# Performance work log

Hardware: AMD Instinct MI355X
Metric: run time of the kernel (lower is better)

Reference implementation:

```python
import jax, jax.numpy as jnp
from jax import lax
import numpy as np

B, W, V, E, H = 512, 40, 12000, 512, 512


def setup_inputs() -> dict:
    key = jax.random.key(0)
    ks = jax.random.split(key, 9)
    s = 0.05
    ques_vec = jax.random.randint(ks[0], (B, W), 0, V + 1)          # token ids, 0 = pad
    ques_len = jax.random.randint(ks[1], (B,), 1, W + 1)             # valid lengths in [1, W]
    lookup_W = jax.random.normal(ks[2], (E, V), jnp.float32) * s     # nn.Linear(vocab, emb).weight
    wih0 = jax.random.normal(ks[3], (2, 4 * H, E), jnp.float32) * s  # [dir, 4H, in]
    whh0 = jax.random.normal(ks[4], (2, 4 * H, H), jnp.float32) * s
    b0 = jax.random.normal(ks[5], (2, 2, 4 * H), jnp.float32) * s    # [dir, {b_ih,b_hh}, 4H]
    wih1 = jax.random.normal(ks[6], (2, 4 * H, 2 * H), jnp.float32) * s
    whh1 = jax.random.normal(ks[7], (2, 4 * H, H), jnp.float32) * s
    b1 = jax.random.normal(ks[8], (2, 2, 4 * H), jnp.float32) * s
    return {"ques_vec": ques_vec, "ques_len": ques_len, "lookup_W": lookup_W,
            "wih0": wih0, "whh0": whh0, "b0": b0,
            "wih1": wih1, "whh1": whh1, "b1": b1}


def _lstm_dir(x, wih, whh, b, reverse):
    # x: [B, T, D]; PyTorch gate order i, f, g, o
    Hc = whh.shape[1]
    xg = jnp.einsum('btd,gd->btg', x, wih) + b[0] + b[1]  # [B, T, 4H]
    xs = jnp.swapaxes(xg, 0, 1)                            # [T, B, 4H]
    if reverse:
        xs = xs[::-1]

    def step(carry, g_t):
        h, c = carry
        g = g_t + h @ whh.T
        i, f, gg, o = jnp.split(g, 4, axis=-1)
        c = jax.nn.sigmoid(f) * c + jax.nn.sigmoid(i) * jnp.tanh(gg)
        h = jax.nn.sigmoid(o) * jnp.tanh(c)
        return (h, c), h

    h0 = jnp.zeros((x.shape[0], Hc), x.dtype)
    _, hs = lax.scan(step, (h0, h0), xs)
    if reverse:
        hs = hs[::-1]
    return jnp.swapaxes(hs, 0, 1)  # [B, T, H]


def _bilstm(x, wih, whh, b):
    fwd = _lstm_dir(x, wih[0], whh[0], b[0], False)
    bwd = _lstm_dir(x, wih[1], whh[1], b[1], True)
    return jnp.concatenate([fwd, bwd], axis=-1)  # [B, T, 2H]


def reference(ques_vec, ques_len, lookup_W, wih0, whh0, b0, wih1, whh1, b1):
    # one-hot over vocab+1 with column 0 dropped == gather with id 0 -> zero vector
    table = jnp.concatenate([jnp.zeros((1, E), lookup_W.dtype), lookup_W.T], axis=0)  # [V+1, E]
    emb = jnp.tanh(table[ques_vec])          # [B, W, E] (dropout=0 -> identity)
    h = _bilstm(emb, wih0, whh0, b0)         # layer 0
    h = _bilstm(h, wih1, whh1, b1)           # layer 1 -> [B, W, 2H]
    # scatter-mask bmm == select hidden state at timestep ques_len-1
    idx = (ques_len - 1)[:, None, None]
    return jnp.take_along_axis(h, idx, axis=1).reshape(ques_vec.shape[0], -1)  # [B, 2H]
```

## Files before the change

### kernel.cpp

```cpp
#include <hip/hip_runtime.h>
#include <hip/hip_bf16.h>
#include <stdint.h>

#define NB 512
#define NW 40
#define NE 512
#define NH 512
#define NV 12000
#define G4 2048

typedef unsigned short u16;
typedef unsigned int u32;
typedef unsigned long long u64;
typedef __attribute__((ext_vector_type(8))) short short8;
typedef __attribute__((ext_vector_type(4))) float f32x4;

__device__ __forceinline__ unsigned short f2bf(float f) {
  unsigned int u = __float_as_uint(f);
  u += 0x7FFF + ((u >> 16) & 1);
  return (unsigned short)(u >> 16);
}
__device__ __forceinline__ float bf2f(unsigned short b) {
  return __uint_as_float(((unsigned int)b) << 16);
}
__device__ __forceinline__ float loadIn(const void* p, long i, int bf) {
  return bf ? bf2f(((const u16*)p)[i]) : ((const float*)p)[i];
}
__device__ __forceinline__ float fast_tanh(float x) {
  float ax = __builtin_fabsf(x);
  float t = 1.f - 2.f * __builtin_amdgcn_rcpf(__expf(ax + ax) + 1.f);
  return __builtin_copysignf(t, x);
}
__device__ __forceinline__ float sigm(float x) {
  return __builtin_amdgcn_rcpf(1.f + __expf(-x));
}

__global__ void detect_kernel(const u16* p, int* flag) {
  __shared__ int cnt;
  int i = threadIdx.x;
  if (i == 0) cnt = 0;
  __syncthreads();
  unsigned short u = p[2 * (i * 1001)];
  int e = (u >> 7) & 0xFF;
  if (e >= 100 && e <= 126) atomicAdd(&cnt, 1);
  __syncthreads();
  if (i == 0) *flag = (cnt >= 32) ? 1 : 0;
}

__global__ void table_kernel(const void* lookup, const int* flag, u16* tableT) {
  __shared__ float tile[64][65];
  int bf = *flag;
  int v0 = blockIdx.x * 64, e0 = blockIdx.y * 64;
  int tx = threadIdx.x, ty = threadIdx.y;
#pragma unroll
  for (int r = 0; r < 16; ++r) {
    int e = r * 4 + ty, v = tx;
    if (v0 + v < NV)
      tile[e][v] = tanhf(loadIn(lookup, (long)(e0 + e) * NV + v0 + v, bf));
  }
  __syncthreads();
#pragma unroll
  for (int r = 0; r < 16; ++r) {
    int v = r * 4 + ty, e = tx;
    if (v0 + v < NV)
      tableT[(long)(v0 + v) * NE + e0 + e] = f2bf(tile[e][v]);
  }
}

__global__ void pack_kernel(const void* wih0, const void* whh0, const void* b0,
                            const void* wih1, const void* whh1, const void* b1,
                            const int* flag, u16* Wc0, u16* Wc1, float* bsum,
                            u16* G) {
  const long N0 = 2L * G4 * 1024, N1 = 2L * G4 * 1536;
  const long NB2 = 2L * 2 * G4;
  long idx = (long)blockIdx.x * 256 + threadIdx.x;
  int bf = *flag;
  if (idx < N0) {
    int d = (int)(idx / (G4 * 1024));
    int rem = (int)(idx % (long)(G4 * 1024));
    int g = rem / 1024, k = rem % 1024;
    float v = (k < 512) ? loadIn(wih0, ((long)d * G4 + g) * 512 + k, bf)
                        : loadIn(whh0, ((long)d * G4 + g) * 512 + (k - 512), bf);
    Wc0[idx] = f2bf(v);
  } else if (idx < N0 + N1) {
    long i2 = idx - N0;
    int d = (int)(i2 / (G4 * 1536));
    int rem = (int)(i2 % (long)(G4 * 1536));
    int g = rem / 1536, k = rem % 1536;
    float v = (k < 1024) ? loadIn(wih1, ((long)d * G4 + g) * 1024 + k, bf)
                         : loadIn(whh1, ((long)d * G4 + g) * 512 + (k - 1024), bf);
    Wc1[i2] = f2bf(v);
  } else if (idx < N0 + N1 + NB2) {
    long i3 = idx - N0 - N1;
    int layer = (int)(i3 / (2 * G4));
    int d = (int)((i3 / G4) & 1);
    int g = (int)(i3 % G4);
    const void* bb = layer ? b1 : b0;
    float v = loadIn(bb, (long)d * 2 * G4 + g, bf) +
              loadIn(bb, (long)d * 2 * G4 + G4 + g, bf);
    bsum[i3] = v;
  } else if (idx < N0 + N1 + NB2 + 4096) {
    int n = (int)(idx - N0 - N1 - NB2);
    int d = n >> 11, loc = n & 2047;
    int colb = loc >> 7, rr = loc & 127;
    int jn = rr >> 2, g = rr & 3;
    int grow = g * 512 + colb * 32 + jn;
    float v = loadIn(b0, (long)d * 2 * G4 + grow, bf) +
              loadIn(b0, (long)d * 2 * G4 + G4 + grow, bf);
    G[n] = f2bf(v);
  }
}

__global__ void zero_bar(unsigned int* bar) {
  bar[blockIdx.x * 256 + threadIdx.x] = 0u;
}

__global__ __launch_bounds__(256, 3) void g_gemm(
    const u16* __restrict__ tableT, const u16* __restrict__ Wc,
    const float* __restrict__ bsumL, u16* __restrict__ G) {
  __shared__ __align__(16) char lds[32768];
  const int tid = threadIdx.x;
  const int lane = tid & 63, wv = tid >> 6;
  const int wm = wv & 1, wn = wv >> 1;
  const int col = lane & 15, quad = lane >> 4;
  const int bx = blockIdx.x >> 5;
  const int by = blockIdx.x & 31;
  const int tb0 = bx * 128;
  const int d = by >> 4, colb = by & 15, j0 = colb * 32;

  f32x4 zero = {0.f, 0.f, 0.f, 0.f};
  f32x4 acc[4][4];
#pragma unroll
  for (int i = 0; i < 4; ++i)
#pragma unroll
    for (int j = 0; j < 4; ++j) acc[i][j] = zero;

  for (int it = 0; it < 8; ++it) {
    int k0 = it << 6;
#pragma unroll
    for (int p = 0; p < 8; ++p) {
      int c = p * 256 + tid;
      const u16* gsrc;
      if (c < 1024) {
        int r = c >> 3, sl = c & 7;
        int kk = k0 + ((sl * 8) ^ ((r & 7) << 3));
        gsrc = tableT + (long)(tb0 + r) * 512 + kk;
      } else {
        int cb = c - 1024;
        int r = cb >> 3, sl = cb & 7;
        int kk = k0 + ((sl * 8) ^ ((r & 7) << 3));
        int grow = (r >> 5) * 512 + j0 + (r & 31);
        gsrc = Wc + ((long)d * G4 + grow) * 1024 + kk;
      }
      __builtin_amdgcn_global_load_lds(
          (const __attribute__((address_space(1))) void*)(const void*)gsrc,
          (__attribute__((address_space(3))) void*)(lds + p * 4096 + wv * 1024),
          16, 0, 0);
    }
    __syncthreads();
    const u16* As = (const u16*)lds;
    const u16* Bs = (const u16*)(lds + 16384);
#pragma unroll
    for (int ks = 0; ks < 2; ++ks) {
      short8 afr[4], bfr[4];
#pragma unroll
      for (int mf = 0; mf < 4; ++mf) {
        int rm = wm * 64 + mf * 16 + col;
        int sl = (ks * 32 + quad * 8) ^ ((rm & 7) << 3);
        afr[mf] = *(const short8*)(As + rm * 64 + sl);
      }
#pragma unroll
      for (int nf = 0; nf < 4; ++nf) {
        int br = wn * 64 + nf * 16 + col;
        int sl = (ks * 32 + quad * 8) ^ ((br & 7) << 3);
        bfr[nf] = *(const short8*)(Bs + br * 64 + sl);
      }
#pragma unroll
      for (int mf = 0; mf < 4; ++mf)
#pragma unroll
        for (int nf = 0; nf < 4; ++nf)
          acc[mf][nf] = __builtin_amdgcn_mfma_f32_16x16x32_bf16(
              afr[mf], bfr[nf], acc[mf][nf], 0, 0, 0);
    }
    __syncthreads();
  }

  float bias[4];
#pragma unroll
  for (int nf = 0; nf < 4; ++nf) {
    int n = wn * 64 + nf * 16 + col;
    bias[nf] = bsumL[d * G4 + (n >> 5) * 512 + j0 + (n & 31)];
  }
#pragma unroll
  for (int mf = 0; mf < 4; ++mf)
#pragma unroll
    for (int nf = 0; nf < 4; ++nf) {
      int n = wn * 64 + nf * 16 + col;
      int g = n >> 5, jn = n & 31;
#pragma unroll
      for (int r = 0; r < 4; ++r) {
        int m = wm * 64 + mf * 16 + quad * 4 + r;
        int v = tb0 + m;
        if (v < NV)
          G[(long)(v + 1) * 4096 + ((d * 16 + colb) << 7) + jn * 4 + g] =
              f2bf(acc[mf][nf][r] + bias[nf]);
      }
    }
}

__global__ __launch_bounds__(256, 3) void xg_gemm(
    const u16* __restrict__ X, int Kx, int Kfull, const u16* __restrict__ Wc,
    const float* __restrict__ bsumL, u16* __restrict__ xg) {
  __shared__ __align__(16) char lds[32768];
  const int tid = threadIdx.x;
  const int lane = tid & 63, wv = tid >> 6;
  const int wm = wv & 1, wn = wv >> 1;
  const int col = lane & 15, quad = lane >> 4;
  const int s = blockIdx.x >> 5, w = blockIdx.x & 31;
  const int bx = (s % 40) * 4 + (w & 3);
  const int by = (s / 40) * 8 + (w >> 2);
  const int tb0 = bx * 128;
  const int d = by >> 4, colb = by & 15, j0 = colb * 32;

  f32x4 zero = {0.f, 0.f, 0.f, 0.f};
  f32x4 acc[4][4];
#pragma unroll
  for (int i = 0; i < 4; ++i)
#pragma unroll
    for (int j = 0; j < 4; ++j) acc[i][j] = zero;

  const int iters = Kx >> 6;
  for (int it = 0; it < iters; ++it) {
    int k0 = it << 6;
#pragma unroll
    for (int p = 0; p < 8; ++p) {
      int c = p * 256 + tid;
      const u16* gsrc;
      if (c < 1024) {
        int r = c >> 3, sl = c & 7;
        int kk = k0 + ((sl * 8) ^ ((r & 7) << 3));
        gsrc = X + (long)(tb0 + r) * Kx + kk;
      } else {
        int cb = c - 1024;
        int r = cb >> 3, sl = cb & 7;
        int kk = k0 + ((sl * 8) ^ ((r & 7) << 3));
        int grow = (r >> 5) * 512 + j0 + (r & 31);
        gsrc = Wc + ((long)d * G4 + grow) * Kfull + kk;
      }
      __builtin_amdgcn_global_load_lds(
          (const __attribute__((address_space(1))) void*)(const void*)gsrc,
          (__attribute__((address_space(3))) void*)(lds + p * 4096 + wv * 1024),
          16, 0, 0);
    }
    __syncthreads();
    const u16* As = (const u16*)lds;
    const u16* Bs = (const u16*)(lds + 16384);
#pragma unroll
    for (int ks = 0; ks < 2; ++ks) {
      short8 afr[4], bfr[4];
#pragma unroll
      for (int mf = 0; mf < 4; ++mf) {
        int rm = wm * 64 + mf * 16 + col;
        int sl = (ks * 32 + quad * 8) ^ ((rm & 7) << 3);
        afr[mf] = *(const short8*)(As + rm * 64 + sl);
      }
#pragma unroll
      for (int nf = 0; nf < 4; ++nf) {
        int br = wn * 64 + nf * 16 + col;
        int sl = (ks * 32 + quad * 8) ^ ((br & 7) << 3);
        bfr[nf] = *(const short8*)(Bs + br * 64 + sl);
      }
#pragma unroll
      for (int mf = 0; mf < 4; ++mf)
#pragma unroll
        for (int nf = 0; nf < 4; ++nf)
          acc[mf][nf] = __builtin_amdgcn_mfma_f32_16x16x32_bf16(
              afr[mf], bfr[nf], acc[mf][nf], 0, 0, 0);
    }
    __syncthreads();
  }

  float bias[4];
#pragma unroll
  for (int nf = 0; nf < 4; ++nf) {
    int n = wn * 64 + nf * 16 + col;
    bias[nf] = bsumL[d * G4 + (n >> 5) * 512 + j0 + (n & 31)];
  }
#pragma unroll
  for (int mf = 0; mf < 4; ++mf)
#pragma unroll
    for (int nf = 0; nf < 4; ++nf) {
      int n = wn * 64 + nf * 16 + col;
      int g = n >> 5, jn = n & 31;
#pragma unroll
      for (int r = 0; r < 4; ++r) {
        int m = wm * 64 + mf * 16 + quad * 4 + r;
        int tb = tb0 + m, t = tb >> 9, b = tb & 511;
        long oi = ((((long)t * 2 + d) * 16 + colb) * 512 + b) * 128 + jn * 4 + g;
        xg[oi] = f2bf(acc[mf][nf][r] + bias[nf]);
      }
    }
}

__global__ __launch_bounds__(256, 1) void lstm_pers(
    const u16* __restrict__ xg, const int* __restrict__ qv,
    const u16* __restrict__ Wc, int Kfull, int Kx, u16* __restrict__ hbuf,
    u16* __restrict__ h0cat, void* __restrict__ outp,
    const int* __restrict__ qlen, const int* __restrict__ flag,
    unsigned int* bar, int layer) {
  __shared__ __align__(16) char lds[163840];
  const int tid = threadIdx.x;
  const int lane = tid & 63, wv = tid >> 6;
  const int wm = wv & 1, wn = wv >> 1;
  const int col = lane & 15, quad = lane >> 4;
  const int l = blockIdx.x;
  const int colid = l & 31, mi = l >> 5;
  const int colb = colid & 15, j0 = colb * 32, d = colid >> 4;
  const int m0 = mi * 64;
  const int gid = l >> 4;

#pragma unroll
  for (int p = 0; p < 32; ++p) {
    int c = p * 256 + tid;
    int row = c >> 6, rem = c & 63;
    int kc = rem >> 3, sl = rem & 7;
    int grow = (row >> 5) * 512 + j0 + (row & 31);
    int gk = Kx + kc * 64 + ((sl * 8) ^ ((row & 7) << 3));
    const u16* gsrc = Wc + ((long)d * G4 + grow) * Kfull + gk;
    __builtin_amdgcn_global_load_lds(
        (const __attribute__((address_space(1))) void*)(const void*)gsrc,
        (__attribute__((address_space(3))) void*)(lds + p * 4096 + wv * 1024),
        16, 0, 0);
  }
  const u16* Bs = (const u16*)lds;
  char* hstg = lds + 131072;
  u16* hLDS = (u16*)hstg;

  float creg[2][4];
#pragma unroll
  for (int i = 0; i < 2; ++i)
#pragma unroll
    for (int r = 0; r < 4; ++r) creg[i][r] = 0.f;
  const int isbf = *flag;
  f32x4 zero = {0.f, 0.f, 0.f, 0.f};

  __syncthreads();

#pragma unroll 1
  for (int t = 0; t < NW; ++t) {
    const int tq = d ? (NW - 1 - t) : t;

    ushort4 xgv[2][4];
    if (layer == 0) {
#pragma unroll
      for (int mf = 0; mf < 2; ++mf)
#pragma unroll
        for (int r = 0; r < 4; ++r) {
          int m = wm * 32 + mf * 16 + quad * 4 + r;
          int q = qv[(m0 + m) * NW + tq];
          xgv[mf][r] = *(const ushort4*)(xg + (long)q * 4096 +
                                         ((d * 16 + colb) << 7) +
                                         (wn * 16 + col) * 4);
        }
    } else {
      const u16* xgt =
          xg + ((((long)tq * 2 + d) * 16 + colb) * 512 + m0) * 128;
#pragma unroll
      for (int mf = 0; mf < 2; ++mf)
#pragma unroll
        for (int r = 0; r < 4; ++r) {
          int m = wm * 32 + mf * 16 + quad * 4 + r;
          xgv[mf][r] = *(const ushort4*)(xgt + m * 128 + (wn * 16 + col) * 4);
        }
    }

    f32x4 acc[2][4];
#pragma unroll
    for (int i = 0; i < 2; ++i)
#pragma unroll
      for (int j = 0; j < 4; ++j) acc[i][j] = zero;

    if (t > 0) {
      if (wv == 0) {
        u32* sp = bar + gid * 16 + (lane & 15);
        while (__ballot((int)(__hip_atomic_load(sp, __ATOMIC_RELAXED,
                                                __HIP_MEMORY_SCOPE_AGENT) <
                              (u32)t)))
          __builtin_amdgcn_s_sleep(1);
      }
      __syncthreads();

      const u16* hp =
          hbuf + ((t - 1) & 1) * (2L * NB * NH) + ((long)d * NB + m0) * NH;
      auto stageH = [&](int half) {
#pragma unroll
        for (int p = 0; p < 8; ++p) {
          int c = p * 256 + tid;
          int row = c >> 5, slot = c & 31;
          int kk = half * 256 + (slot >> 3) * 64 +
                   (((slot & 7) * 8) ^ ((row & 7) << 3));
          const u16* gsrc = hp + (long)row * NH + kk;
          __builtin_amdgcn_global_load_lds(
              (const __attribute__((address_space(1))) void*)(const void*)gsrc,
              (__attribute__((address_space(3))) void*)(hstg + p * 4096 +
                                                        wv * 1024),
              16, 0, 16 );
        }
      };
      const u16* As = (const u16*)hstg;
#pragma unroll 1
      for (int half = 0; half < 2; ++half) {
        stageH(half);
        __syncthreads();
#pragma unroll
        for (int ks = 0; ks < 8; ++ks) {
          const int ksub = ks * 32 + quad * 8;
          short8 afr[2];
#pragma unroll
          for (int mf = 0; mf < 2; ++mf) {
            int rm = wm * 32 + mf * 16 + col;
            afr[mf] = *(const short8*)(As + rm * 256 + (ksub & ~63) +
                                       ((ksub & 63) ^ ((rm & 7) << 3)));
          }
          const int kc = half * 256 + ksub;
#pragma unroll
          for (int g = 0; g < 4; ++g) {
            int br = g * 32 + wn * 16 + col;
            int slb = (kc & 63) ^ ((br & 7) << 3);
            short8 bfr = *(const short8*)(Bs + br * 512 + (kc & ~63) + slb);
#pragma unroll
            for (int mf = 0; mf < 2; ++mf)
              acc[mf][g] = __builtin_amdgcn_mfma_f32_16x16x32_bf16(
                  afr[mf], bfr, acc[mf][g], 0, 0, 0);
          }
        }
        __syncthreads();
      }
    }

#pragma unroll
    for (int mf = 0; mf < 2; ++mf)
#pragma unroll
      for (int r = 0; r < 4; ++r) {
        int m = wm * 32 + mf * 16 + quad * 4 + r;
        const u16* xv = (const u16*)&xgv[mf][r];
        float gi = acc[mf][0][r] + bf2f(xv[0]);
        float gf = acc[mf][1][r] + bf2f(xv[1]);
        float gg = acc[mf][2][r] + bf2f(xv[2]);
        float go = acc[mf][3][r] + bf2f(xv[3]);
        float si = sigm(gi);
        float sf = sigm(gf);
        float so = sigm(go);
        float cn = sf * creg[mf][r] + si * fast_tanh(gg);
        float h = so * fast_tanh(cn);
        creg[mf][r] = cn;
        hLDS[m * 32 + wn * 16 + col] = f2bf(h);
        if (layer == 1 && !isbf) {
          int bg = m0 + m;
          if (qlen[bg] - 1 == tq)
            ((float*)outp)[(long)bg * (2 * NH) + d * NH + j0 + wn * 16 + col] =
                h;
        }
      }
    __syncthreads();

    u16* hnxt = hbuf + (t & 1) * (2L * NB * NH);
    u32 hw[4];
    int bgp[4], jgp[4];
#pragma unroll
    for (int p = 0; p < 4; ++p) {
      int c = p * 256 + tid;
      int m = c >> 4, pr = c & 15;
      hw[p] = ((const u32*)hLDS)[m * 16 + pr];
      bgp[p] = m0 + m;
      jgp[p] = j0 + pr * 2;
      __hip_atomic_store(
          (u32*)(hnxt + ((long)d * NB + bgp[p]) * NH + jgp[p]), hw[p],
          __ATOMIC_RELAXED, __HIP_MEMORY_SCOPE_AGENT);
    }

    if (t < NW - 1) {
      __syncthreads();
      if (tid == 0)
        __hip_atomic_store(bar + gid * 16 + colb, (u32)(t + 1),
                           __ATOMIC_RELAXED, __HIP_MEMORY_SCOPE_AGENT);
    }

#pragma unroll
    for (int p = 0; p < 4; ++p) {
      if (layer == 0) {
        *(u32*)(h0cat + ((long)tq * NB + bgp[p]) * (2 * NH) + d * NH +
                jgp[p]) = hw[p];
      } else if (isbf && qlen[bgp[p]] - 1 == tq) {
        *(u32*)((u16*)outp + (long)bgp[p] * (2 * NH) + d * NH + jgp[p]) =
            hw[p];
      }
    }
  }
}

extern "C" void kernel_launch(void* const* d_in, const int* in_sizes, int n_in,
                              void* d_out, int out_size, void* d_ws,
                              size_t ws_size, hipStream_t stream) {
  const int* qv = (const int*)d_in[0];
  const int* ql = (const int*)d_in[1];
  const void* lookup = d_in[2];
  const void* wih0 = d_in[3];
  const void* whh0 = d_in[4];
  const void* b0 = d_in[5];
  const void* wih1 = d_in[6];
  const void* whh1 = d_in[7];
  const void* b1 = d_in[8];

  char* ws = (char*)d_ws;
  size_t off = 0;
  int* flag = (int*)ws;                 off += 256;
  unsigned int* bar = (unsigned int*)(ws + off); off += 8192;
  float* bsum = (float*)(ws + off);     off += 2L * 2 * G4 * 4;
  u16* Wc0 = (u16*)(ws + off);          off += 2L * G4 * 1024 * 2;
  u16* Wc1 = (u16*)(ws + off);          off += 2L * G4 * 1536 * 2;
  u16* hbuf = (u16*)(ws + off);         off += 2L * 2 * NB * NH * 2;
  u16* h0cat = (u16*)(ws + off);        off += (size_t)NW * NB * 2 * NH * 2;
  u16* xg = (u16*)(ws + off);           off += (size_t)NW * 2 * 16 * 512 * 128 * 2;
  u16* tableT = h0cat;
  u16* G = xg;

  detect_kernel<<<1, 64, 0, stream>>>((const u16*)lookup, flag);
  table_kernel<<<dim3(188, 8), dim3(64, 4), 0, stream>>>(lookup, flag, tableT);
  {
    long total = 2L * G4 * 1024 + 2L * G4 * 1536 + 2L * 2 * G4 + 4096;
    int blocks = (int)((total + 255) / 256);
    pack_kernel<<<blocks, 256, 0, stream>>>(wih0, whh0, b0, wih1, whh1, b1,
                                            flag, Wc0, Wc1, bsum, G);
  }

  g_gemm<<<94 * 32, 256, 0, stream>>>(tableT, Wc0, bsum, G);
  zero_bar<<<8, 256, 0, stream>>>(bar);
  lstm_pers<<<256, 256, 0, stream>>>(G, qv, Wc0, 1024, 512, hbuf, h0cat,
                                     d_out, ql, flag, bar, 0);
  xg_gemm<<<5120, 256, 0, stream>>>(h0cat, 1024, 1536, Wc1, bsum + 2 * G4, xg);
  zero_bar<<<8, 256, 0, stream>>>(bar);
  lstm_pers<<<256, 256, 0, stream>>>(xg, qv, Wc1, 1536, 1024, hbuf, h0cat,
                                     d_out, ql, flag, bar, 1);
}
```

Before: 853.6 us.

## Keep first K-quarter of Whh in registers and stage full h tile at once

Moves the first 128 K-columns of the recurrent weight slice into per-wave registers and keeps only the remaining 384 columns in LDS, which frees LDS space. The freed space lets the whole 64x512 h tile be staged in one pass instead of two halves. That removes one stage-then-barrier round per timestep and lets the whole K loop run unrolled. The cost is 64 extra VGPRs per thread for the weight fragments, which raises register pressure and spill risk.

```diff
diff --git a/kernel.cpp b/kernel.cpp
--- a/kernel.cpp
+++ b/kernel.cpp
@@ -320,21 +320,30 @@
   const int gid = l >> 4;
 
 #pragma unroll
-  for (int p = 0; p < 32; ++p) {
+  for (int p = 0; p < 24; ++p) {
     int c = p * 256 + tid;
-    int row = c >> 6, rem = c & 63;
-    int kc = rem >> 3, sl = rem & 7;
+    int cc = c >> 10, row = (c >> 3) & 127, sl = c & 7;
     int grow = (row >> 5) * 512 + j0 + (row & 31);
-    int gk = Kx + kc * 64 + ((sl * 8) ^ ((row & 7) << 3));
+    int gk = Kx + 128 + cc * 64 + ((sl * 8) ^ ((row & 7) << 3));
     const u16* gsrc = Wc + ((long)d * G4 + grow) * Kfull + gk;
     __builtin_amdgcn_global_load_lds(
         (const __attribute__((address_space(1))) void*)(const void*)gsrc,
         (__attribute__((address_space(3))) void*)(lds + p * 4096 + wv * 1024),
         16, 0, 0);
   }
-  const u16* Bs = (const u16*)lds;
-  char* hstg = lds + 131072;
+  const u16* WhhB = (const u16*)lds;
+  char* hstg = lds + 98304;
   u16* hLDS = (u16*)hstg;
+
+  short8 breg[4][4];
+#pragma unroll
+  for (int g = 0; g < 4; ++g) {
+    int grow = g * 512 + j0 + wn * 16 + col;
+    const u16* wp = Wc + ((long)d * G4 + grow) * Kfull + Kx;
+#pragma unroll
+    for (int c4 = 0; c4 < 4; ++c4)
+      breg[g][c4] = *(const short8*)(wp + c4 * 32 + quad * 8);
+  }
 
   float creg[2][4];
 #pragma unroll
@@ -392,50 +401,49 @@
 
       const u16* hp =
           hbuf + ((t - 1) & 1) * (2L * NB * NH) + ((long)d * NB + m0) * NH;
-      auto stageH = [&](int half) {
-#pragma unroll
-        for (int p = 0; p < 8; ++p) {
-          int c = p * 256 + tid;
-          int row = c >> 5, slot = c & 31;
-          int kk = half * 256 + (slot >> 3) * 64 +
-                   (((slot & 7) * 8) ^ ((row & 7) << 3));
-          const u16* gsrc = hp + (long)row * NH + kk;
-          __builtin_amdgcn_global_load_lds(
-              (const __attribute__((address_space(1))) void*)(const void*)gsrc,
-              (__attribute__((address_space(3))) void*)(hstg + p * 4096 +
-                                                        wv * 1024),
-              16, 0, 16 );
+#pragma unroll
+      for (int p = 0; p < 16; ++p) {
+        int c = p * 256 + tid;
+        int row = c >> 6, slot = c & 63;
+        int kk = (slot >> 3) * 64 + (((slot & 7) * 8) ^ ((row & 7) << 3));
+        const u16* gsrc = hp + (long)row * NH + kk;
+        __builtin_amdgcn_global_load_lds(
+            (const __attribute__((address_space(1))) void*)(const void*)gsrc,
+            (__attribute__((address_space(3))) void*)(hstg + p * 4096 +
+                                                      wv * 1024),
+            16, 0, 16 );
+      }
+      __syncthreads();
+
+      const u16* As = (const u16*)hstg;
+#pragma unroll
+      for (int ks = 0; ks < 16; ++ks) {
+        const int ksub = ks * 32 + quad * 8;
+        short8 afr[2];
+#pragma unroll
+        for (int mf = 0; mf < 2; ++mf) {
+          int rm = wm * 32 + mf * 16 + col;
+          afr[mf] = *(const short8*)(As + rm * 512 + (ksub & ~63) +
+                                     ((ksub & 63) ^ ((rm & 7) << 3)));
         }
-      };
-      const u16* As = (const u16*)hstg;
-#pragma unroll 1
-      for (int half = 0; half < 2; ++half) {
-        stageH(half);
-        __syncthreads();
-#pragma unroll
-        for (int ks = 0; ks < 8; ++ks) {
-          const int ksub = ks * 32 + quad * 8;
-          short8 afr[2];
-#pragma unroll
-          for (int mf = 0; mf < 2; ++mf) {
-            int rm = wm * 32 + mf * 16 + col;
-            afr[mf] = *(const short8*)(As + rm * 256 + (ksub & ~63) +
-                                       ((ksub & 63) ^ ((rm & 7) << 3)));
+#pragma unroll
+        for (int g = 0; g < 4; ++g) {
+          short8 bfr;
+          if (ks < 4) {
+            bfr = breg[g][ks];
+          } else {
+            int br = g * 32 + wn * 16 + col;
+            int kp = ksub - 128;
+            bfr = *(const short8*)(WhhB + (kp >> 6) * 8192 + br * 64 +
+                                   ((kp & 63) ^ ((br & 7) << 3)));
           }
-          const int kc = half * 256 + ksub;
-#pragma unroll
-          for (int g = 0; g < 4; ++g) {
-            int br = g * 32 + wn * 16 + col;
-            int slb = (kc & 63) ^ ((br & 7) << 3);
-            short8 bfr = *(const short8*)(Bs + br * 512 + (kc & ~63) + slb);
-#pragma unroll
-            for (int mf = 0; mf < 2; ++mf)
-              acc[mf][g] = __builtin_amdgcn_mfma_f32_16x16x32_bf16(
-                  afr[mf], bfr, acc[mf][g], 0, 0, 0);
-          }
+#pragma unroll
+          for (int mf = 0; mf < 2; ++mf)
+            acc[mf][g] = __builtin_amdgcn_mfma_f32_16x16x32_bf16(
+                afr[mf], bfr, acc[mf][g], 0, 0, 0);
         }
-        __syncthreads();
-      }
+      }
+      __syncthreads();
     }
 
 #pragma unroll
```

Result: faster. 832.5 us (-2.5%).
